# Optimization experiments

Hardware: AMD Instinct MI355X
Metric: run time of the kernel (lower is better)

The kernel has to match this reference:

```python
import jax, jax.numpy as jnp
import numpy as np

BN_EPS = 1e-5
K = 3  # k_size


def _unfold(x, k):
    # torch F.unfold with padding=k//2, stride=1, viewed as (B, C, k*k, H, W).
    # Kernel positions are row-major (i slow, j fast), matching torch layout.
    p = k // 2
    B, C, H, W = x.shape
    xp = jnp.pad(x, ((0, 0), (0, 0), (p, p), (p, p)))
    pats = jnp.stack([xp[:, :, i:i + H, j:j + W]
                      for i in range(k) for j in range(k)], axis=2)
    return pats  # (B, C, k*k, H, W)


def _conv1x1(x, w, b):
    # w: (C_out, C_in), x: (B, C_in, H, W)
    return jnp.einsum('oc,bchw->bohw', w, x) + b[None, :, None, None]


def _bn(x, gamma, beta, mean, var):
    inv = gamma / jnp.sqrt(var + BN_EPS)
    return x * inv[None, :, None, None] + (beta - mean * inv)[None, :, None, None]


def setup_inputs() -> dict:
    key = jax.random.key(0)
    ks = jax.random.split(key, 12)
    B, C, H, W = 8, 256, 64, 64
    s = lambda k_, *sh: jax.random.normal(k_, sh, dtype=jnp.float32) * 0.05
    return {
        'x': jax.random.normal(ks[0], (B, C, H, W), dtype=jnp.float32),
        # feature_embedding: Conv2d(C, C, 1) + BN
        'w_embed': s(ks[1], C, C), 'b_embed': jnp.zeros((C,), jnp.float32),
        'bn1_gamma': jnp.ones((C,), jnp.float32), 'bn1_beta': jnp.zeros((C,), jnp.float32),
        'bn1_mean': jnp.zeros((C,), jnp.float32), 'bn1_var': jnp.ones((C,), jnp.float32),
        # enhance: Conv2d(2C, C, 1) + BN
        'w_enh': s(ks[2], C, 2 * C), 'b_enh': jnp.zeros((C,), jnp.float32),
        'bn2_gamma': jnp.ones((C,), jnp.float32), 'bn2_beta': jnp.zeros((C,), jnp.float32),
        'bn2_mean': jnp.zeros((C,), jnp.float32), 'bn2_var': jnp.ones((C,), jnp.float32),
        # weight_gen: Conv2d(2C, C//4, 1) -> ReLU -> Conv2d(C//4, C, 1) -> Sigmoid
        'w_g1': s(ks[3], C // 4, 2 * C), 'b_g1': jnp.zeros((C // 4,), jnp.float32),
        'w_g2': s(ks[4], C, C // 4), 'b_g2': jnp.zeros((C,), jnp.float32),
    }


def reference(x, w_embed, b_embed, bn1_gamma, bn1_beta, bn1_mean, bn1_var,
              w_enh, b_enh, bn2_gamma, bn2_beta, bn2_mean, bn2_var,
              w_g1, b_g1, w_g2, b_g2):
    B, C, H, W = x.shape
    # ---- feature embedding: 1x1 conv + BN (eval) + ReLU
    fe = jax.nn.relu(_bn(_conv1x1(x, w_embed, b_embed),
                         bn1_gamma, bn1_beta, bn1_mean, bn1_var))
    # ---- region similarity: cosine(center pixel, each kxk neighbor) over C
    pats = _unfold(fe, K)                       # (B, C, k2, H, W)
    sim = jnp.einsum('bchw,bckhw->bkhw', fe, pats)
    norm_c = jnp.sqrt(jnp.sum(fe * fe, axis=1))             # (B, H, W)
    norm_p = jnp.sqrt(jnp.sum(pats * pats, axis=1))         # (B, k2, H, W)
    sim = sim / (norm_c[:, None] * norm_p + 1e-7)
    sim = jax.nn.softmax(sim, axis=1)                       # over k2 window
    # ---- dynamic feature aggregation on original x
    xpats = _unfold(x, K)                                   # (B, C, k2, H, W)
    agg = jnp.einsum('bckhw,bkhw->bchw', xpats, sim)
    enhanced = jax.nn.relu(_bn(_conv1x1(jnp.concatenate([x, agg], axis=1), w_enh, b_enh),
                               bn2_gamma, bn2_beta, bn2_mean, bn2_var))
    # ---- output modulation (SE-style gating)
    pooled = jnp.mean(jnp.concatenate([x, enhanced], axis=1), axis=(2, 3), keepdims=True)
    h = jax.nn.relu(_conv1x1(pooled, w_g1, b_g1))
    weights = jax.nn.sigmoid(_conv1x1(h, w_g2, b_g2))       # (B, C, 1, 1)
    return x + weights * enhanced
```

## Files before the change

### kernel.cpp

```cpp
#include <hip/hip_runtime.h>
#include <math.h>

typedef unsigned short u16;
typedef unsigned int   u32;
typedef __attribute__((ext_vector_type(8))) short short8;
typedef __attribute__((ext_vector_type(4))) short s16x4;
typedef __attribute__((ext_vector_type(4))) float f32x4;

#define OFS_XB   0ul
#define OFS_W1B  8388608ul
#define OFS_W2B  8421376ul
#define OFS_B1   8486912ul
#define OFS_B2   8487168ul
#define OFS_POOL 8487424ul
#define OFS_ENH  8491520ul
#define OFS_XC   16880128ul

__device__ __forceinline__ u16 f2bf(float x) {
    union { float f; u32 u; } v; v.f = x;
    u32 r = v.u + 0x7fffu + ((v.u >> 16) & 1u);
    return (u16)(r >> 16);
}
__device__ __forceinline__ float bf2f(u16 h) {
    union { u32 u; float f; } v; v.u = ((u32)h) << 16;
    return v.f;
}
__device__ __forceinline__ void ld_g2l_16(u16* l, const u16* g) {
    __builtin_amdgcn_global_load_lds(
        (const __attribute__((address_space(1))) u32*)g,
        (__attribute__((address_space(3))) u32*)l,
        16, 0, 0);
}

__global__ __launch_bounds__(256) void k_cvt(
    const float* __restrict__ x, u16* __restrict__ xb, u16* __restrict__ xc,
    float* __restrict__ pool,
    const float* __restrict__ w1, const float* __restrict__ b1,
    const float* __restrict__ g1, const float* __restrict__ be1,
    const float* __restrict__ m1, const float* __restrict__ v1,
    const float* __restrict__ w2, const float* __restrict__ b2,
    const float* __restrict__ g2, const float* __restrict__ be2,
    const float* __restrict__ m2, const float* __restrict__ v2,
    u16* __restrict__ w1b, u16* __restrict__ w2b,
    float* __restrict__ b1f, float* __restrict__ b2f)
{
    __shared__ float tile[64][65];
    const int t = threadIdx.x;
    const int id = blockIdx.x;
    if (id < 1) {
        const float4 z = {0.f, 0.f, 0.f, 0.f};
#pragma unroll
        for (int i = 0; i < 4; ++i) ((float4*)pool)[i * 256 + t] = z;
        return;
    }
    if (id < 771) {
        int idx = (id - 1) * 256 + t;
        if (idx < 65536) {
            int o = idx >> 8;
            float inv = g1[o] * rsqrtf(v1[o] + 1e-5f);
            w1b[idx] = f2bf(w1[idx] * inv);
        } else if (idx < 196608) {
            int j = idx - 65536;
            int o = j >> 9;
            float inv = g2[o] * rsqrtf(v2[o] + 1e-5f);
            w2b[j] = f2bf(w2[j] * inv);
        } else if (idx < 196864) {
            int o = idx - 196608;
            float inv = g1[o] * rsqrtf(v1[o] + 1e-5f);
            b1f[o] = b1[o] * inv + be1[o] - m1[o] * inv;
        } else if (idx < 197120) {
            int o = idx - 196864;
            float inv = g2[o] * rsqrtf(v2[o] + 1e-5f);
            b2f[o] = b2[o] * inv + be2[o] - m2[o] * inv;
        }
        return;
    }
    const int cid = id - 771;
    const int pt = cid & 63, ct = (cid >> 6) & 3, b = cid >> 8;
    const float* src = x + (((size_t)(b * 256 + ct * 64)) << 12) + pt * 64;
#pragma unroll
    for (int i = 0; i < 16; ++i) {
        int idx = i * 256 + t;
        int cl = idx >> 6, pl = idx & 63;
        tile[cl][pl] = src[((size_t)cl << 12) + pl];
    }
    __syncthreads();
#pragma unroll
    for (int i = 0; i < 8; ++i) {
        int idx = i * 256 + t;
        int pl = idx >> 5, c2 = idx & 31;
        int cl = c2 * 2;
        u32 lo = f2bf(tile[cl][pl]);
        u32 hi = f2bf(tile[cl + 1][pl]);
        *(u32*)(xb + (((size_t)(b * 4096 + pt * 64 + pl)) << 9) + ct * 64 + cl) = lo | (hi << 16);
    }
#pragma unroll
    for (int i = 0; i < 8; ++i) {
        int idx = i * 256 + t;
        int cl = idx >> 5, pl2 = (idx & 31) * 2;
        u32 lo = f2bf(tile[cl][pl2]);
        u32 hi = f2bf(tile[cl][pl2 + 1]);
        *(u32*)(xc + (((size_t)(b * 256 + ct * 64 + cl)) << 12) + pt * 64 + pl2) = lo | (hi << 16);
    }
    if (t < 64) {
        float s = 0.f;
#pragma unroll
        for (int i = 0; i < 64; ++i) s += tile[t][i];
        atomicAdd(&pool[(b << 9) + ct * 64 + t], s * (1.f / 4096.f));
    }
}

template<int KIN, bool OUTT, bool DOPOOL>
__global__ __launch_bounds__(256) void k_gemm(
    const u16* __restrict__ xb, const u16* __restrict__ Wb,
    const float* __restrict__ biasf, void* __restrict__ outp,
    float* __restrict__ poolp)
{
    __shared__ __align__(16) u16 Wl[4096];
    __shared__ __align__(16) u16 Xl[4096];
    __shared__ __align__(16) u16 ct[OUTT ? 16384 : 4];
    __shared__ float sbias[128];
    const int t = threadIdx.x;
    const int lane = t & 63;
    const int wv = t >> 6;
    const int id = blockIdx.x;
    const int p_blk = (((id >> 4) << 3) | (id & 7)) * 128;
    const int o_blk = ((id >> 3) & 1) * 128;
    const int owg = (wv & 1) * 4;
    const int pwg = (wv >> 1) * 4;
    const int r16 = lane & 15, q = lane >> 4;
    if (t < 128) sbias[t] = biasf[o_blk + t];

    f32x4 acc[4][4];
#pragma unroll
    for (int i = 0; i < 4; ++i)
#pragma unroll
        for (int j = 0; j < 4; ++j) acc[i][j] = (f32x4){0.f, 0.f, 0.f, 0.f};

    for (int kc = 0; kc < KIN / 32; ++kc) {
        const int kk = kc * 32 + q * 8;
#pragma unroll
        for (int s = 0; s < 4; ++s) {
            const int bi = wv * 4 + s;
            const u16* g;
            u16* l;
            if (bi < 8) {
                g = Wb + (size_t)(o_blk + bi * 16 + r16) * KIN + kk;
                l = Wl + bi * 512;
            } else {
                g = xb + (((size_t)(p_blk + (bi - 8) * 16 + r16)) << 9) + kk;
                l = Xl + (bi - 8) * 512;
            }
            ld_g2l_16(l, g);
        }
        __syncthreads();
        short8 af[4], bf[4];
#pragma unroll
        for (int i = 0; i < 4; ++i) af[i] = *(const short8*)(Wl + (owg + i) * 512 + lane * 8);
#pragma unroll
        for (int j = 0; j < 4; ++j) bf[j] = *(const short8*)(Xl + (pwg + j) * 512 + lane * 8);
#pragma unroll
        for (int i = 0; i < 4; ++i)
#pragma unroll
            for (int j = 0; j < 4; ++j)
                acc[i][j] = __builtin_amdgcn_mfma_f32_16x16x32_bf16(af[i], bf[j], acc[i][j], 0, 0, 0);
        __syncthreads();
    }

    float bia[4][4];
#pragma unroll
    for (int i = 0; i < 4; ++i)
#pragma unroll
        for (int r = 0; r < 4; ++r) bia[i][r] = sbias[owg * 16 + i * 16 + q * 4 + r];
    const int bidx = p_blk >> 12;

    if (OUTT) {
#pragma unroll
        for (int i = 0; i < 4; ++i) {
#pragma unroll
            for (int j = 0; j < 4; ++j) {
                const int px_l = pwg * 16 + j * 16 + r16;
#pragma unroll
                for (int rp = 0; rp < 2; ++rp) {
                    const int r0 = rp * 2;
                    const int o_l = owg * 16 + i * 16 + q * 4 + r0;
                    const float v0 = fmaxf(acc[i][j][r0] + bia[i][r0], 0.f);
                    const float v1 = fmaxf(acc[i][j][r0 + 1] + bia[i][r0 + 1], 0.f);
                    const u32 pk = (u32)f2bf(v0) | ((u32)f2bf(v1) << 16);
                    *(u32*)((char*)ct + px_l * 256 + ((o_l * 2) ^ ((px_l & 7) << 4))) = pk;
                }
            }
        }
        __syncthreads();
        u16* feT = (u16*)outp;
#pragma unroll
        for (int it = 0; it < 16; ++it) {
            const int idx = it * 256 + t;
            const int px_l = idx >> 5, cd = idx & 31;
            s16x4 v = *(const s16x4*)((char*)ct + px_l * 256 + ((cd * 8) ^ ((px_l & 7) << 4)));
            *(s16x4*)(feT + (((size_t)(bidx * 4096 + (p_blk & 4095) + px_l)) << 8) + o_blk + cd * 4) = v;
        }
        return;
    }

    const int pin0 = (p_blk & 4095) + pwg * 16 + r16;
#pragma unroll
    for (int i = 0; i < 4; ++i) {
#pragma unroll
        for (int r = 0; r < 4; ++r) {
            const int o = o_blk + owg * 16 + i * 16 + q * 4 + r;
            const size_t rowb = ((size_t)(bidx * 256 + o)) << 12;
            float ps = 0.f;
#pragma unroll
            for (int j = 0; j < 4; ++j) {
                float v = fmaxf(acc[i][j][r] + bia[i][r], 0.f);
                const size_t oi = rowb + pin0 + j * 16;
                ((u16*)outp)[oi] = f2bf(v);
                ps += v;
            }
            if (DOPOOL) {
                ps += __shfl_down(ps, 8, 16);
                ps += __shfl_down(ps, 4, 16);
                ps += __shfl_down(ps, 2, 16);
                ps += __shfl_down(ps, 1, 16);
                if (r16 == 0)
                    atomicAdd(&poolp[(bidx << 9) + 256 + o], ps * (1.f / 4096.f));
            }
        }
    }
}

__global__ __launch_bounds__(256) void k_simagg(
    const u16* __restrict__ fe, const u16* __restrict__ xb, u16* __restrict__ xbo)
{
    __shared__ float red[16][17][13];
    __shared__ float redh[2][3][16];
    __shared__ float redsum[11][16];
    __shared__ float nrmh[2][3];
    __shared__ float ws9[9][16];
    const int t = threadIdx.x;
    const int id = blockIdx.x;
    const int b = id & 7, h = (id >> 3) & 63, q = id >> 9;
    const int px0 = q * 16;
    const int rows[3] = {h > 0 ? h - 1 : 0, h, h < 63 ? h + 1 : 63};

    {
        const int pxl = t >> 4, cs = t & 15;
        const int px = px0 + pxl;
        const int pxL = px > 0 ? px - 1 : 0, pxR = px < 63 ? px + 1 : 63;
        const int pxs[3] = {pxL, px, pxR};
        const u16* feb = fe + (((size_t)(b * 4096)) << 8) + cs * 8;
        float cvec[16];
        float dot[9];
        float nn0 = 0.f, nn2 = 0.f;
        {
            const u16* p = feb + (((size_t)(rows[1] * 64 + px)) << 8);
            short8 v0 = *(const short8*)p;
            short8 v1 = *(const short8*)(p + 128);
            float s = 0.f;
#pragma unroll
            for (int u = 0; u < 8; ++u) {
                float f0 = bf2f((u16)v0[u]), f1 = bf2f((u16)v1[u]);
                cvec[u] = f0; cvec[8 + u] = f1;
                s = fmaf(f0, f0, s); s = fmaf(f1, f1, s);
            }
            dot[4] = s;
        }
#pragma unroll
        for (int r = 0; r < 3; ++r) {
#pragma unroll
            for (int j = 0; j < 3; ++j) {
                if (r == 1 && j == 1) continue;
                const int k = r * 3 + j;
                const u16* p = feb + (((size_t)(rows[r] * 64 + pxs[j])) << 8);
                short8 v0 = *(const short8*)p;
                short8 v1 = *(const short8*)(p + 128);
                float s = 0.f, qq = 0.f;
#pragma unroll
                for (int u = 0; u < 8; ++u) {
                    float f0 = bf2f((u16)v0[u]), f1 = bf2f((u16)v1[u]);
                    s = fmaf(cvec[u], f0, s);
                    s = fmaf(cvec[8 + u], f1, s);
                    if (j == 1) { qq = fmaf(f0, f0, qq); qq = fmaf(f1, f1, qq); }
                }
                dot[k] = s;
                if (j == 1) { if (r == 0) nn0 = qq; else nn2 = qq; }
            }
        }
#pragma unroll
        for (int k = 0; k < 9; ++k) red[cs][pxl][k] = dot[k];
        red[cs][pxl][9] = nn0;
        red[cs][pxl][10] = nn2;
    }
    if (t < 96) {
        const int side = t / 48, rr = (t % 48) / 16, cs = t & 15;
        const int pxh = side ? (px0 + 16 < 64 ? px0 + 16 : 63) : (px0 > 0 ? px0 - 1 : 0);
        const u16* p = fe + (((size_t)(b * 4096 + rows[rr] * 64 + pxh)) << 8) + cs * 8;
        short8 v0 = *(const short8*)p;
        short8 v1 = *(const short8*)(p + 128);
        float qq = 0.f;
#pragma unroll
        for (int u = 0; u < 8; ++u) {
            float f0 = bf2f((u16)v0[u]), f1 = bf2f((u16)v1[u]);
            qq = fmaf(f0, f0, qq); qq = fmaf(f1, f1, qq);
        }
        redh[side][rr][cs] = qq;
    }
    __syncthreads();
    if (t < 176) {
        const int pxl = t & 15, k = t >> 4;
        float s = 0.f;
#pragma unroll
        for (int g = 0; g < 16; ++g) s += red[g][pxl][k];
        redsum[k][pxl] = s;
    } else if (t < 182) {
        const int u_ = t - 176;
        const int side = u_ / 3, rr = u_ % 3;
        float s = 0.f;
#pragma unroll
        for (int g = 0; g < 16; ++g) s += redh[side][rr][g];
        nrmh[side][rr] = s;
    }
    __syncthreads();
    if (t < 16) {
        const int w = px0 + t;
        const float nc = sqrtf(redsum[4][t]);
        float sv[9], mk[9];
#pragma unroll
        for (int di = -1; di <= 1; ++di) {
#pragma unroll
            for (int dj = -1; dj <= 1; ++dj) {
                const int k = (di + 1) * 3 + (dj + 1);
                const int hn = h + di, wn = w + dj;
                const float mask = (hn >= 0 && hn < 64 && wn >= 0 && wn < 64) ? 1.f : 0.f;
                const int j = t + dj;
                const int ridx = di + 1;
                float nk;
                if (j < 0)        nk = nrmh[0][ridx];
                else if (j > 15)  nk = nrmh[1][ridx];
                else              nk = (ridx == 0) ? redsum[9][j]
                                     : (ridx == 1) ? redsum[4][j] : redsum[10][j];
                mk[k] = mask;
                sv[k] = mask * redsum[k][t] / (nc * sqrtf(nk) + 1e-7f);
            }
        }
        float mx = sv[0];
#pragma unroll
        for (int k = 1; k < 9; ++k) mx = fmaxf(mx, sv[k]);
        float e[9], sum = 0.f;
#pragma unroll
        for (int k = 0; k < 9; ++k) { e[k] = expf(sv[k] - mx); sum += e[k]; }
        const float rs = 1.f / sum;
#pragma unroll
        for (int k = 0; k < 9; ++k) ws9[k][t] = mk[k] * e[k] * rs;
    }
    __syncthreads();
    const int cd = t & 63, pg = t >> 6;
    const u16* xbb = xb + (((size_t)(b * 4096)) << 9) + cd * 4;
    u16* orow = xbo + (((size_t)(b * 4096 + h * 64)) << 9) + 256 + cd * 4;
#pragma unroll
    for (int pi = 0; pi < 4; ++pi) {
        const int pxl = pg * 4 + pi;
        const int px = px0 + pxl;
        const int pL = px > 0 ? px - 1 : 0, pR = px < 63 ? px + 1 : 63;
        const int pxs2[3] = {pL, px, pR};
        float m9[9];
#pragma unroll
        for (int k = 0; k < 9; ++k) m9[k] = ws9[k][pxl];
        float a0 = 0.f, a1 = 0.f, a2 = 0.f, a3 = 0.f;
#pragma unroll
        for (int r = 0; r < 3; ++r) {
#pragma unroll
            for (int j = 0; j < 3; ++j) {
                const float m = m9[r * 3 + j];
                s16x4 v = *(const s16x4*)(xbb + (((size_t)(rows[r] * 64 + pxs2[j])) << 9));
                a0 = fmaf(bf2f((u16)v[0]), m, a0);
                a1 = fmaf(bf2f((u16)v[1]), m, a1);
                a2 = fmaf(bf2f((u16)v[2]), m, a2);
                a3 = fmaf(bf2f((u16)v[3]), m, a3);
            }
        }
        s16x4 sv4;
        sv4[0] = (short)f2bf(a0); sv4[1] = (short)f2bf(a1);
        sv4[2] = (short)f2bf(a2); sv4[3] = (short)f2bf(a3);
        *(s16x4*)(orow + ((size_t)px << 9)) = sv4;
    }
}

__global__ __launch_bounds__(256) void k_final(
    const u16* __restrict__ xc, const u16* __restrict__ enh,
    const float* __restrict__ pool,
    const float* __restrict__ wg1, const float* __restrict__ bg1,
    const float* __restrict__ wg2, const float* __restrict__ bg2,
    float* __restrict__ out)
{
    __shared__ float pl[512];
    __shared__ float hpart[4][64];
    __shared__ float hb[64];
    __shared__ float sg[256];
    const int t = threadIdx.x;
    const int id = blockIdx.x;
    const int b = id & 7, cg = id >> 3;
    pl[t] = pool[b * 512 + t];
    pl[t + 256] = pool[b * 512 + 256 + t];
    __syncthreads();
    {
        const int o = t & 63, seg = t >> 6;
        float s = 0.f;
        const float* wr_ = wg1 + o * 512 + seg * 128;
        const float* pr_ = pl + seg * 128;
#pragma unroll 4
        for (int j = 0; j < 128; ++j) s = fmaf(wr_[j], pr_[j], s);
        hpart[seg][o] = s;
    }
    __syncthreads();
    if (t < 64)
        hb[t] = fmaxf(hpart[0][t] + hpart[1][t] + hpart[2][t] + hpart[3][t] + bg1[t], 0.f);
    __syncthreads();
    {
        float s2 = bg2[t];
        const float* w2 = wg2 + t * 64;
#pragma unroll 4
        for (int j = 0; j < 64; ++j) s2 = fmaf(w2[j], hb[j], s2);
        sg[t] = 1.f / (1.f + expf(-s2));
    }
    __syncthreads();
    const int cl = t >> 6, l = t & 63;
    const int c = cg * 4 + cl;
    const float gt = sg[c];
    const u16* xp = xc + (((size_t)(b * 256 + c)) << 12);
    const u16* ep = enh + (((size_t)(b * 256 + c)) << 12);
    float*     op = out + (((size_t)(b * 256 + c)) << 12);
#pragma unroll
    for (int ch = 0; ch < 8; ++ch) {
        const int base = ch * 512 + l * 8;
        short8 ev = *(const short8*)(ep + base);
        short8 xv = *(const short8*)(xp + base);
        float4 o0, o1;
        o0.x = fmaf(gt, bf2f((u16)ev[0]), bf2f((u16)xv[0]));
        o0.y = fmaf(gt, bf2f((u16)ev[1]), bf2f((u16)xv[1]));
        o0.z = fmaf(gt, bf2f((u16)ev[2]), bf2f((u16)xv[2]));
        o0.w = fmaf(gt, bf2f((u16)ev[3]), bf2f((u16)xv[3]));
        o1.x = fmaf(gt, bf2f((u16)ev[4]), bf2f((u16)xv[4]));
        o1.y = fmaf(gt, bf2f((u16)ev[5]), bf2f((u16)xv[5]));
        o1.z = fmaf(gt, bf2f((u16)ev[6]), bf2f((u16)xv[6]));
        o1.w = fmaf(gt, bf2f((u16)ev[7]), bf2f((u16)xv[7]));
        *(float4*)(op + base) = o0;
        *(float4*)(op + base + 4) = o1;
    }
}

extern "C" void kernel_launch(void* const* d_in, const int* in_sizes, int n_in,
                              void* d_out, int out_size, void* d_ws, size_t ws_size,
                              hipStream_t stream)
{
    const float* x       = (const float*)d_in[0];
    const float* w_embed = (const float*)d_in[1];
    const float* b_embed = (const float*)d_in[2];
    const float* g1      = (const float*)d_in[3];
    const float* be1     = (const float*)d_in[4];
    const float* m1      = (const float*)d_in[5];
    const float* v1      = (const float*)d_in[6];
    const float* w_enh   = (const float*)d_in[7];
    const float* b_enh   = (const float*)d_in[8];
    const float* g2      = (const float*)d_in[9];
    const float* be2     = (const float*)d_in[10];
    const float* m2      = (const float*)d_in[11];
    const float* v2      = (const float*)d_in[12];
    const float* w_g1    = (const float*)d_in[13];
    const float* b_g1    = (const float*)d_in[14];
    const float* w_g2    = (const float*)d_in[15];
    const float* b_g2    = (const float*)d_in[16];
    float* ws  = (float*)d_ws;
    float* out = (float*)d_out;

    u16*   xb   = (u16*)(ws + OFS_XB);
    u16*   w1b  = (u16*)(ws + OFS_W1B);
    u16*   w2b  = (u16*)(ws + OFS_W2B);
    float* b1f  = ws + OFS_B1;
    float* b2f  = ws + OFS_B2;
    float* pool = ws + OFS_POOL;
    u16*   enh  = (u16*)(ws + OFS_ENH);
    u16*   xc   = (u16*)(ws + OFS_XC);
    u16*   fe   = (u16*)d_out;

    k_cvt<<<dim3(2819), dim3(256), 0, stream>>>(
        x, xb, xc, pool,
        w_embed, b_embed, g1, be1, m1, v1,
        w_enh, b_enh, g2, be2, m2, v2, w1b, w2b, b1f, b2f);
    k_gemm<256, true, false><<<dim3(512), dim3(256), 0, stream>>>(xb, w1b, b1f, (void*)fe, nullptr);
    k_simagg<<<dim3(2048), dim3(256), 0, stream>>>(fe, xb, xb);
    k_gemm<512, false, true><<<dim3(512), dim3(256), 0, stream>>>(xb, w2b, b2f, (void*)enh, pool);
    k_final<<<dim3(512), dim3(256), 0, stream>>>(xc, enh, pool, w_g1, b_g1, w_g2, b_g2, out);
}
```

Measured before the change: 201.4 us.

## Compute per-pixel feature norms in embedding GEMM epilogue instead of sim kernel

The embedding GEMM epilogue now accumulates squared fe values per pixel and atomically adds them into a new global norm buffer, which k_cvt zeroes. The similarity kernel reads neighbor norms from that buffer, so it no longer recomputes squared norms for the neighbor rows or the halo pixels. This drops redundant loads and FMAs and frees shared memory there. A launch-bounds occupancy hint is also added. The cost is extra atomics in the GEMM, and the norms come from fp32 values rather than the bf16-rounded fe, a slight numeric difference.

```diff
diff --git a/kernel.cpp b/kernel.cpp
--- a/kernel.cpp
+++ b/kernel.cpp
@@ -13,8 +13,9 @@
 #define OFS_B1   8486912ul
 #define OFS_B2   8487168ul
 #define OFS_POOL 8487424ul
-#define OFS_ENH  8491520ul
-#define OFS_XC   16880128ul
+#define OFS_NRM  8491520ul
+#define OFS_ENH  8524288ul
+#define OFS_XC   16912896ul
 
 __device__ __forceinline__ u16 f2bf(float x) {
     union { float f; u32 u; } v; v.f = x;
@@ -34,7 +35,7 @@
 
 __global__ __launch_bounds__(256) void k_cvt(
     const float* __restrict__ x, u16* __restrict__ xb, u16* __restrict__ xc,
-    float* __restrict__ pool,
+    float* __restrict__ pool, float* __restrict__ nrm,
     const float* __restrict__ w1, const float* __restrict__ b1,
     const float* __restrict__ g1, const float* __restrict__ be1,
     const float* __restrict__ m1, const float* __restrict__ v1,
@@ -47,14 +48,18 @@
     __shared__ float tile[64][65];
     const int t = threadIdx.x;
     const int id = blockIdx.x;
-    if (id < 1) {
+    if (id < 33) {
         const float4 z = {0.f, 0.f, 0.f, 0.f};
-#pragma unroll
-        for (int i = 0; i < 4; ++i) ((float4*)pool)[i * 256 + t] = z;
+        if (id == 0) {
+#pragma unroll
+            for (int i = 0; i < 4; ++i) ((float4*)pool)[i * 256 + t] = z;
+        } else {
+            ((float4*)(nrm + (id - 1) * 1024))[t] = z;
+        }
         return;
     }
-    if (id < 771) {
-        int idx = (id - 1) * 256 + t;
+    if (id < 803) {
+        int idx = (id - 33) * 256 + t;
         if (idx < 65536) {
             int o = idx >> 8;
             float inv = g1[o] * rsqrtf(v1[o] + 1e-5f);
@@ -75,7 +80,7 @@
         }
         return;
     }
-    const int cid = id - 771;
+    const int cid = id - 803;
     const int pt = cid & 63, ct = (cid >> 6) & 3, b = cid >> 8;
     const float* src = x + (((size_t)(b * 256 + ct * 64)) << 12) + pt * 64;
 #pragma unroll
@@ -114,7 +119,7 @@
 __global__ __launch_bounds__(256) void k_gemm(
     const u16* __restrict__ xb, const u16* __restrict__ Wb,
     const float* __restrict__ biasf, void* __restrict__ outp,
-    float* __restrict__ poolp)
+    float* __restrict__ poolp, float* __restrict__ nrmp)
 {
     __shared__ __align__(16) u16 Wl[4096];
     __shared__ __align__(16) u16 Xl[4096];
@@ -175,6 +180,7 @@
     const int bidx = p_blk >> 12;
 
     if (OUTT) {
+        float psn[4] = {0.f, 0.f, 0.f, 0.f};
 #pragma unroll
         for (int i = 0; i < 4; ++i) {
 #pragma unroll
@@ -186,10 +192,19 @@
                     const int o_l = owg * 16 + i * 16 + q * 4 + r0;
                     const float v0 = fmaxf(acc[i][j][r0] + bia[i][r0], 0.f);
                     const float v1 = fmaxf(acc[i][j][r0 + 1] + bia[i][r0 + 1], 0.f);
+                    psn[j] = fmaf(v0, v0, fmaf(v1, v1, psn[j]));
                     const u32 pk = (u32)f2bf(v0) | ((u32)f2bf(v1) << 16);
                     *(u32*)((char*)ct + px_l * 256 + ((o_l * 2) ^ ((px_l & 7) << 4))) = pk;
                 }
             }
+        }
+#pragma unroll
+        for (int j = 0; j < 4; ++j) {
+            float ps = psn[j];
+            ps += __shfl_down(ps, 32);
+            ps += __shfl_down(ps, 16);
+            if (q == 0)
+                atomicAdd(&nrmp[bidx * 4096 + (p_blk & 4095) + pwg * 16 + j * 16 + r16], ps);
         }
         __syncthreads();
         u16* feT = (u16*)outp;
@@ -230,13 +245,12 @@
     }
 }
 
-__global__ __launch_bounds__(256) void k_simagg(
-    const u16* __restrict__ fe, const u16* __restrict__ xb, u16* __restrict__ xbo)
+__global__ __launch_bounds__(256, 6) void k_simagg(
+    const u16* __restrict__ fe, const float* __restrict__ nrm,
+    const u16* __restrict__ xb, u16* __restrict__ xbo)
 {
-    __shared__ float red[16][17][13];
-    __shared__ float redh[2][3][16];
-    __shared__ float redsum[11][16];
-    __shared__ float nrmh[2][3];
+    __shared__ float red[16][17][9];
+    __shared__ float redsum[9][16];
     __shared__ float ws9[9][16];
     const int t = threadIdx.x;
     const int id = blockIdx.x;
@@ -252,7 +266,6 @@
         const u16* feb = fe + (((size_t)(b * 4096)) << 8) + cs * 8;
         float cvec[16];
         float dot[9];
-        float nn0 = 0.f, nn2 = 0.f;
         {
             const u16* p = feb + (((size_t)(rows[1] * 64 + px)) << 8);
             short8 v0 = *(const short8*)p;
@@ -275,55 +288,30 @@
                 const u16* p = feb + (((size_t)(rows[r] * 64 + pxs[j])) << 8);
                 short8 v0 = *(const short8*)p;
                 short8 v1 = *(const short8*)(p + 128);
-                float s = 0.f, qq = 0.f;
+                float s = 0.f;
 #pragma unroll
                 for (int u = 0; u < 8; ++u) {
-                    float f0 = bf2f((u16)v0[u]), f1 = bf2f((u16)v1[u]);
-                    s = fmaf(cvec[u], f0, s);
-                    s = fmaf(cvec[8 + u], f1, s);
-                    if (j == 1) { qq = fmaf(f0, f0, qq); qq = fmaf(f1, f1, qq); }
+                    s = fmaf(cvec[u], bf2f((u16)v0[u]), s);
+                    s = fmaf(cvec[8 + u], bf2f((u16)v1[u]), s);
                 }
                 dot[k] = s;
-                if (j == 1) { if (r == 0) nn0 = qq; else nn2 = qq; }
             }
         }
 #pragma unroll
         for (int k = 0; k < 9; ++k) red[cs][pxl][k] = dot[k];
-        red[cs][pxl][9] = nn0;
-        red[cs][pxl][10] = nn2;
-    }
-    if (t < 96) {
-        const int side = t / 48, rr = (t % 48) / 16, cs = t & 15;
-        const int pxh = side ? (px0 + 16 < 64 ? px0 + 16 : 63) : (px0 > 0 ? px0 - 1 : 0);
-        const u16* p = fe + (((size_t)(b * 4096 + rows[rr] * 64 + pxh)) << 8) + cs * 8;
-        short8 v0 = *(const short8*)p;
-        short8 v1 = *(const short8*)(p + 128);
-        float qq = 0.f;
-#pragma unroll
-        for (int u = 0; u < 8; ++u) {
-            float f0 = bf2f((u16)v0[u]), f1 = bf2f((u16)v1[u]);
-            qq = fmaf(f0, f0, qq); qq = fmaf(f1, f1, qq);
-        }
-        redh[side][rr][cs] = qq;
-    }
-    __syncthreads();
-    if (t < 176) {
+    }
+    __syncthreads();
+    if (t < 144) {
         const int pxl = t & 15, k = t >> 4;
         float s = 0.f;
 #pragma unroll
         for (int g = 0; g < 16; ++g) s += red[g][pxl][k];
         redsum[k][pxl] = s;
-    } else if (t < 182) {
-        const int u_ = t - 176;
-        const int side = u_ / 3, rr = u_ % 3;
-        float s = 0.f;
-#pragma unroll
-        for (int g = 0; g < 16; ++g) s += redh[side][rr][g];
-        nrmh[side][rr] = s;
     }
     __syncthreads();
     if (t < 16) {
         const int w = px0 + t;
+        const float* nb = nrm + b * 4096;
         const float nc = sqrtf(redsum[4][t]);
         float sv[9], mk[9];
 #pragma unroll
@@ -333,13 +321,8 @@
                 const int k = (di + 1) * 3 + (dj + 1);
                 const int hn = h + di, wn = w + dj;
                 const float mask = (hn >= 0 && hn < 64 && wn >= 0 && wn < 64) ? 1.f : 0.f;
-                const int j = t + dj;
-                const int ridx = di + 1;
-                float nk;
-                if (j < 0)        nk = nrmh[0][ridx];
-                else if (j > 15)  nk = nrmh[1][ridx];
-                else              nk = (ridx == 0) ? redsum[9][j]
-                                     : (ridx == 1) ? redsum[4][j] : redsum[10][j];
+                const int wc = wn < 0 ? 0 : (wn > 63 ? 63 : wn);
+                const float nk = nb[rows[di + 1] * 64 + wc];
                 mk[k] = mask;
                 sv[k] = mask * redsum[k][t] / (nc * sqrtf(nk) + 1e-7f);
             }
@@ -480,16 +463,17 @@
     float* b1f  = ws + OFS_B1;
     float* b2f  = ws + OFS_B2;
     float* pool = ws + OFS_POOL;
+    float* nrm  = ws + OFS_NRM;
     u16*   enh  = (u16*)(ws + OFS_ENH);
     u16*   xc   = (u16*)(ws + OFS_XC);
     u16*   fe   = (u16*)d_out;
 
-    k_cvt<<<dim3(2819), dim3(256), 0, stream>>>(
-        x, xb, xc, pool,
+    k_cvt<<<dim3(2851), dim3(256), 0, stream>>>(
+        x, xb, xc, pool, nrm,
         w_embed, b_embed, g1, be1, m1, v1,
         w_enh, b_enh, g2, be2, m2, v2, w1b, w2b, b1f, b2f);
-    k_gemm<256, true, false><<<dim3(512), dim3(256), 0, stream>>>(xb, w1b, b1f, (void*)fe, nullptr);
-    k_simagg<<<dim3(2048), dim3(256), 0, stream>>>(fe, xb, xb);
-    k_gemm<512, false, true><<<dim3(512), dim3(256), 0, stream>>>(xb, w2b, b2f, (void*)enh, pool);
+    k_gemm<256, true, false><<<dim3(512), dim3(256), 0, stream>>>(xb, w1b, b1f, (void*)fe, nullptr, nrm);
+    k_simagg<<<dim3(2048), dim3(256), 0, stream>>>(fe, nrm, xb, xb);
+    k_gemm<512, false, true><<<dim3(512), dim3(256), 0, stream>>>(xb, w2b, b2f, (void*)enh, pool, nullptr);
     k_final<<<dim3(512), dim3(256), 0, stream>>>(xc, enh, pool, w_g1, b_g1, w_g2, b_g2, out);
 }
```

New measurement: 232.6 us. 15.5% more time.
